# Kernel tuning notes

Measured on AMD Instinct MI355X. Metric: run time of the kernel, lower is better.

Reference implementation:

```python
import jax, jax.numpy as jnp
import numpy as np

K, D, Q, N = 32, 256, 16, 4096
LOG2PI = float(np.log(2.0 * np.pi))


def setup_inputs() -> dict:
    key = jax.random.key(0)
    k1, k2, k3, k4 = jax.random.split(key, 4)
    X = jax.random.normal(k1, (N, D), dtype=jnp.float32)
    log_pi = jnp.full((K,), -np.log(K), dtype=jnp.float32)  # uniform mixture weights
    mu = 0.1 * jax.random.normal(k2, (K, D), dtype=jnp.float32)
    Lambda = 0.1 * jax.random.normal(k3, (K, D, Q), dtype=jnp.float32)
    log_psi = np.float32(np.log(0.01)) + 0.1 * jax.random.normal(k4, (K, D), dtype=jnp.float32)
    return {"X": X, "log_pi": log_pi, "mu": mu, "Lambda": Lambda, "log_psi": log_psi}


def reference(X, log_pi, mu, Lambda, log_psi):
    """MFA e_step: per-component Gaussian log-prob with C_k = L_k L_k^T + diag(psi_k) + jitter.
    Returns (log_resp_norm [N,K], log_likelihood [N]) — same math as the torch loop, batched over K."""
    d = X.shape[1]
    psi = jnp.exp(log_psi) + 1e-6                       # [K,D]
    C = jnp.einsum('kdq,keq->kde', Lambda, Lambda)       # [K,D,D] low-rank part
    C = C + jnp.eye(d, dtype=X.dtype) * (psi + 1e-5)[:, None, :]  # add diag(psi) + 1e-5 jitter
    chol = jnp.linalg.cholesky(C)                        # [K,D,D]
    diff = X[None, :, :] - mu[:, None, :]                # [K,N,D]
    # solve chol @ y = diff^T  (batched lower-triangular solve)
    y = jax.scipy.linalg.solve_triangular(chol, diff.transpose(0, 2, 1), lower=True)  # [K,D,N]
    maha = jnp.sum(y * y, axis=1)                        # [K,N]
    logdet = 2.0 * jnp.sum(jnp.log(jnp.diagonal(chol, axis1=1, axis2=2)), axis=1)  # [K]
    log_prob = -0.5 * (maha + d * LOG2PI + logdet[:, None])  # [K,N]
    log_resps = log_prob.T + log_pi[None, :]             # [N,K]
    log_likelihood = jax.scipy.special.logsumexp(log_resps, axis=1)  # [N]
    log_resp_norm = log_resps - log_likelihood[:, None]
    return log_resp_norm, log_likelihood
```

## Files before the change

### kernel.cpp

```cpp
#include <hip/hip_runtime.h>
#include <math.h>

#define KC 32
#define DD 256
#define QQ 16
#define NPTS 4096
#define NROW 8
#define LOG2PI_F 1.8378770664093453f

typedef unsigned short ushort_t;

#define OFF_U    0
#define OFF_LOGC 512
#define OFF_HB   544

__device__ __forceinline__ ushort_t f2bf(float f) {
    union { float f; unsigned int u; } c; c.f = f;
    unsigned int u = c.u;
    return (ushort_t)((u + 0x7FFFu + ((u >> 16) & 1u)) >> 16);
}
__device__ __forceinline__ float bf2f(ushort_t h) {
    union { unsigned int u; float f; } c; c.u = ((unsigned int)h) << 16;
    return c.f;
}

using short8 = __attribute__((ext_vector_type(8))) short;
using f32x4  = __attribute__((ext_vector_type(4))) float;

#define PSTR 260
__global__ __launch_bounds__(256) void precompute_kernel(
    const float* __restrict__ log_pi, const float* __restrict__ mu,
    const float* __restrict__ Lambda, const float* __restrict__ log_psi,
    float* __restrict__ ws)
{
    __shared__ __align__(16) float sLamT[QQ * PSTR];
    __shared__ __align__(16) float sLhatT[QQ * PSTR];
    __shared__ __align__(16) float sMu[DD];
    __shared__ float sM[QQ * 17];
    __shared__ float sL[QQ * 17];
    __shared__ float sY[QQ * 17];
    __shared__ float sCol[QQ];
    __shared__ float sPart[8];
    __shared__ float sScal[2];

    const int k = blockIdx.x;
    const int tid = threadIdx.x;
    const int lane = tid & 63;
    const int wave = tid >> 6;
    ushort_t* hb = (ushort_t*)(ws + OFF_HB);
    const int d = tid;

    float Psi  = expf(log_psi[k * DD + d]) + 1.1e-5f;
    float vinv = 1.0f / Psi;
    float mud  = mu[k * DD + d];
    float wv   = vinv * mud;
    hb[(512 + k) * DD + d] = f2bf(vinv);
    hb[(544 + k) * DD + d] = f2bf(wv);
    sMu[d] = mud;
    float logPsi = logf(Psi);
    float ckp = wv * mud;

    float lam[QQ];
    const float4* lrow = reinterpret_cast<const float4*>(Lambda + (size_t)(k * DD + d) * QQ);
#pragma unroll
    for (int i = 0; i < 4; ++i) {
        float4 t = lrow[i];
        lam[4 * i + 0] = t.x; lam[4 * i + 1] = t.y;
        lam[4 * i + 2] = t.z; lam[4 * i + 3] = t.w;
    }
#pragma unroll
    for (int q = 0; q < QQ; ++q) {
        float lh = lam[q] * vinv;
        sLamT[q * PSTR + d]  = lam[q];
        sLhatT[q * PSTR + d] = lh;
        hb[(k * QQ + q) * DD + d] = f2bf(lh);
    }

    float r0 = logPsi, r1 = ckp;
#pragma unroll
    for (int off = 32; off >= 1; off >>= 1) {
        r0 += __shfl_down(r0, off);
        r1 += __shfl_down(r1, off);
    }
    if ((tid & 63) == 0) { sPart[wave] = r0; sPart[4 + wave] = r1; }
    __syncthreads();
    if (tid == 0) {
        sScal[0] = sPart[0] + sPart[1] + sPart[2] + sPart[3];
        sScal[1] = sPart[4] + sPart[5] + sPart[6] + sPart[7];
    }

    {
        int q = tid >> 4, r = tid & 15;
        const float4* aq = reinterpret_cast<const float4*>(sLhatT + q * PSTR);
        const float4* br = reinterpret_cast<const float4*>(sLamT + r * PSTR);
        float acc = 0.f;
#pragma unroll
        for (int i = 0; i < DD / 4; ++i) {
            float4 a = aq[i], b = br[i];
            acc += a.x * b.x + a.y * b.y + a.z * b.z + a.w * b.w;
        }
        sM[q * 17 + r] = acc + ((q == r) ? 1.0f : 0.0f);
    }
    __syncthreads();
    if (tid < QQ) {
        const float4* aq = reinterpret_cast<const float4*>(sLhatT + tid * PSTR);
        const float4* bm = reinterpret_cast<const float4*>(sMu);
        float acc = 0.f;
#pragma unroll
        for (int i = 0; i < DD / 4; ++i) {
            float4 a = aq[i], b = bm[i];
            acc += a.x * b.x + a.y * b.y + a.z * b.z + a.w * b.w;
        }
        ws[OFF_U + k * QQ + tid] = acc;
    }

    if (wave == 0 && lane < QQ) {
        const int r = lane;
        float m[QQ], l[QQ];
#pragma unroll
        for (int c = 0; c < QQ; ++c) m[c] = sM[r * 17 + c];
#pragma unroll
        for (int j = 0; j < QQ; ++j) {
            float djj = __shfl(m[j], j);
            float rinv = 1.0f / sqrtf(djj);
            l[j] = m[j] * rinv;
            sCol[r] = l[j];
#pragma unroll
            for (int c = 0; c < QQ; ++c)
                if (c > j) m[c] -= l[j] * sCol[c];
        }
#pragma unroll
        for (int j = 0; j < QQ; ++j) sL[r * 17 + j] = l[j];
        float dl = logf(l[r]);
        dl += __shfl_xor(dl, 1); dl += __shfl_xor(dl, 2);
        dl += __shfl_xor(dl, 4); dl += __shfl_xor(dl, 8);
        if (r == 0) sPart[1] = dl;
    }
    __syncthreads();

    if (wave == 0 && lane < QQ) {
        const int c = lane;
        float y[QQ];
#pragma unroll
        for (int j = 0; j < QQ; ++j) {
            float acc = (j == c) ? 1.0f : 0.0f;
#pragma unroll
            for (int i = 0; i < QQ; ++i)
                if (i < j) acc -= sL[j * 17 + i] * y[i];
            y[j] = acc / sL[j * 17 + j];
        }
#pragma unroll
        for (int j = 0; j < QQ; ++j) sY[j * 17 + c] = y[j];
    }
    __syncthreads();

    {
        int q = tid >> 4, r = tid & 15;
        float acc = 0.f;
#pragma unroll
        for (int j = 0; j < QQ; ++j) acc += sY[j * 17 + q] * sY[j * 17 + r];
        hb[(576 + k) * DD + tid] = f2bf(acc);
    }
    if (tid == 0) {
        float logdet = sScal[0] + 2.0f * sPart[1];
        ws[OFF_LOGC + k] = log_pi[k] - 0.5f * ((float)DD * LOG2PI_F + logdet)
                         - 0.5f * sScal[1];
    }
}

#define SXH 264
#define TSTR 520
#define QSTR 68
#define SRS 36

__global__ __launch_bounds__(512, 2) void main_kernel(
    const float* __restrict__ X, const float* __restrict__ ws,
    float* __restrict__ out)
{
    const int tid  = threadIdx.x;
    const int lane = tid & 63;
    const int wave = tid >> 6;
    const int n0   = blockIdx.x * NROW;
    const ushort_t* hB = (const ushort_t*)(ws + OFF_HB);

    __shared__ __align__(16) ushort_t xh[16 * SXH];
    __shared__ __align__(16) ushort_t sT[NROW * TSTR];
    __shared__ __align__(16) float    sQS[NROW * QSTR];
    __shared__ float sU[512];
    __shared__ float sLogc[KC];
    __shared__ float sR[NROW * SRS];
    __shared__ float sLse[NROW];

    {
        const float4* gx = reinterpret_cast<const float4*>(X + (size_t)n0 * DD);
        int row = tid >> 6, d4 = tid & 63;
        float4 v = gx[tid];
        *reinterpret_cast<ushort4*>(&xh[row * SXH + d4 * 4]) =
            make_ushort4(f2bf(v.x), f2bf(v.y), f2bf(v.z), f2bf(v.w));
        int zr = 8 + (tid >> 6), zc = (tid & 63) * 4;
        *reinterpret_cast<ushort4*>(&xh[zr * SXH + zc]) = make_ushort4(0, 0, 0, 0);
        sU[tid] = ws[OFF_U + tid];
        if (tid < KC) sLogc[tid] = ws[OFF_LOGC + tid];
    }
    __syncthreads();

    {
        const int arow = lane & 15;
        const int quad = lane >> 4;
        short8 a[8];
        const ushort_t* ab = xh + arow * SXH + quad * 8;
#pragma unroll
        for (int ks = 0; ks < 8; ++ks) a[ks] = *reinterpret_cast<const short8*>(ab + ks * 32);

#pragma unroll
        for (int i = 0; i < 4; ++i) {
            const int tile = wave * 4 + i;
            const ushort_t* gB = hB + (size_t)(tile * 16 + arow) * DD + quad * 8;
            f32x4 acc = (f32x4){0.f, 0.f, 0.f, 0.f};
#pragma unroll
            for (int ks = 0; ks < 8; ++ks)
                acc = __builtin_amdgcn_mfma_f32_16x16x32_bf16(
                    a[ks], *reinterpret_cast<const short8*>(gB + ks * 32), acc, 0, 0, 0);
            float uu = sU[tile * 16 + arow];
#pragma unroll
            for (int r = 0; r < 4; ++r) {
                int rr = quad * 4 + r;
                if (rr < NROW) sT[rr * TSTR + tile * 16 + arow] = f2bf(acc[r] - uu);
            }
        }
        if (wave < 4) {
            short8 aa[8];
            if (wave < 2) {
#pragma unroll
                for (int ks = 0; ks < 8; ++ks) {
                    short8 sq;
#pragma unroll
                    for (int e = 0; e < 8; ++e) {
                        float xf = bf2f((ushort_t)a[ks][e]);
                        sq[e] = (short)f2bf(xf * xf);
                    }
                    aa[ks] = sq;
                }
            } else {
#pragma unroll
                for (int ks = 0; ks < 8; ++ks) aa[ks] = a[ks];
            }
            const ushort_t* gB = hB + (size_t)(512 + wave * 16 + arow) * DD + quad * 8;
            f32x4 acc = (f32x4){0.f, 0.f, 0.f, 0.f};
#pragma unroll
            for (int ks = 0; ks < 8; ++ks)
                acc = __builtin_amdgcn_mfma_f32_16x16x32_bf16(
                    aa[ks], *reinterpret_cast<const short8*>(gB + ks * 32), acc, 0, 0, 0);
            const int col = (wave & 1) * 16 + arow + ((wave >> 1) & 1) * 32;
#pragma unroll
            for (int r = 0; r < 4; ++r) {
                int rr = quad * 4 + r;
                if (rr < NROW) sQS[rr * QSTR + col] = acc[r];
            }
        }
    }
    __syncthreads();

    {
        const int half = tid & 1;
        const int row  = (tid >> 1) & 7;
        const int c    = (tid >> 4) & 31;
        float t[16];
        {
            const ushort_t* tp = sT + row * TSTR + c * 16;
            short8 t0 = *reinterpret_cast<const short8*>(tp);
            short8 t1 = *reinterpret_cast<const short8*>(tp + 8);
#pragma unroll
            for (int e = 0; e < 8; ++e) {
                t[e]     = bf2f((ushort_t)t0[e]);
                t[8 + e] = bf2f((ushort_t)t1[e]);
            }
        }
        const ushort_t* mp = hB + (size_t)(576 + c) * DD + half * 128;
        float corr = 0.f;
#pragma unroll
        for (int q = 0; q < 8; ++q) {
            short8 m0 = *reinterpret_cast<const short8*>(mp + q * 16);
            short8 m1 = *reinterpret_cast<const short8*>(mp + q * 16 + 8);
            float inner = 0.f;
#pragma unroll
            for (int e = 0; e < 8; ++e)
                inner += bf2f((ushort_t)m0[e]) * t[e] + bf2f((ushort_t)m1[e]) * t[8 + e];
            corr += t[half * 8 + q] * inner;
        }
        corr += __shfl_xor(corr, 1);
        if (half == 0) {
            float qx = sQS[row * QSTR + c];
            float sx = sQS[row * QSTR + 32 + c];
            sR[row * SRS + c] = sLogc[c] - 0.5f * (qx - 2.0f * sx - corr);
        }
    }
    __syncthreads();

    if (tid < NROW) {
        float m = -INFINITY;
#pragma unroll
        for (int c = 0; c < KC; ++c) m = fmaxf(m, sR[tid * SRS + c]);
        float sum = 0.f;
#pragma unroll
        for (int c = 0; c < KC; ++c) sum += expf(sR[tid * SRS + c] - m);
        float lse = m + logf(sum);
        sLse[tid] = lse;
        out[(size_t)NPTS * KC + n0 + tid] = lse;
    }
    __syncthreads();
    if (tid < NROW * 8) {
        int r = tid >> 3, i = tid & 7;
        float lse = sLse[r];
        float4 v = *reinterpret_cast<const float4*>(sR + r * SRS + i * 4);
        float4 o = make_float4(v.x - lse, v.y - lse, v.z - lse, v.w - lse);
        *reinterpret_cast<float4*>(out + (size_t)(n0 + r) * KC + i * 4) = o;
    }
}

extern "C" void kernel_launch(void* const* d_in, const int* in_sizes, int n_in,
                              void* d_out, int out_size, void* d_ws, size_t ws_size,
                              hipStream_t stream)
{
    (void)in_sizes; (void)n_in; (void)out_size; (void)ws_size;
    const float* X       = (const float*)d_in[0];
    const float* log_pi  = (const float*)d_in[1];
    const float* mu      = (const float*)d_in[2];
    const float* Lambda  = (const float*)d_in[3];
    const float* log_psi = (const float*)d_in[4];
    float* out = (float*)d_out;
    float* ws  = (float*)d_ws;

    precompute_kernel<<<dim3(KC), dim3(256), 0, stream>>>(log_pi, mu, Lambda, log_psi, ws);
    main_kernel<<<dim3(NPTS / NROW), dim3(512), 0, stream>>>(X, ws, out);
}
```

Measured before the change: 94.97 us.

## Process 16 points per block and use MFMA for precompute Gram products

The main kernel now handles 16 rows per block instead of 8, so the 16-row MFMA tiles are fully used rather than half padded with zeros, and the grid is halved. The correction stage loops over two components per thread to cover the doubled work. The precompute kernel stores Lambda, Lambda/psi and mu as bf16 in shared memory and computes the 16x16 Gram matrix and the u vector with MFMA instead of scalar fp32 dot products. This adds bf16 rounding to the precompute and halves the number of blocks, which lowers occupancy and parallelism.

```diff
diff --git a/kernel.cpp b/kernel.cpp
--- a/kernel.cpp
+++ b/kernel.cpp
@@ -5,7 +5,7 @@
 #define DD 256
 #define QQ 16
 #define NPTS 4096
-#define NROW 8
+#define NROW 16
 #define LOG2PI_F 1.8378770664093453f
 
 typedef unsigned short ushort_t;
@@ -27,15 +27,15 @@
 using short8 = __attribute__((ext_vector_type(8))) short;
 using f32x4  = __attribute__((ext_vector_type(4))) float;
 
-#define PSTR 260
+#define HSTR 264
 __global__ __launch_bounds__(256) void precompute_kernel(
     const float* __restrict__ log_pi, const float* __restrict__ mu,
     const float* __restrict__ Lambda, const float* __restrict__ log_psi,
     float* __restrict__ ws)
 {
-    __shared__ __align__(16) float sLamT[QQ * PSTR];
-    __shared__ __align__(16) float sLhatT[QQ * PSTR];
-    __shared__ __align__(16) float sMu[DD];
+    __shared__ __align__(16) ushort_t lamH[QQ * HSTR];
+    __shared__ __align__(16) ushort_t lhatH[QQ * HSTR];
+    __shared__ __align__(16) ushort_t smuH[QQ * HSTR];
     __shared__ float sM[QQ * 17];
     __shared__ float sL[QQ * 17];
     __shared__ float sY[QQ * 17];
@@ -56,24 +56,38 @@
     float wv   = vinv * mud;
     hb[(512 + k) * DD + d] = f2bf(vinv);
     hb[(544 + k) * DD + d] = f2bf(wv);
-    sMu[d] = mud;
+    smuH[d] = f2bf(mud);
     float logPsi = logf(Psi);
     float ckp = wv * mud;
 
-    float lam[QQ];
-    const float4* lrow = reinterpret_cast<const float4*>(Lambda + (size_t)(k * DD + d) * QQ);
+    {
+        const float4* lrow = reinterpret_cast<const float4*>(Lambda + (size_t)(k * DD + d) * QQ);
+#pragma unroll
+        for (int i = 0; i < 4; ++i) {
+            float4 t = lrow[i];
+            float l0 = t.x, l1 = t.y, l2 = t.z, l3 = t.w;
+            int q = 4 * i;
+            lamH[(q + 0) * HSTR + d] = f2bf(l0);
+            lamH[(q + 1) * HSTR + d] = f2bf(l1);
+            lamH[(q + 2) * HSTR + d] = f2bf(l2);
+            lamH[(q + 3) * HSTR + d] = f2bf(l3);
+            ushort_t h0 = f2bf(l0 * vinv), h1 = f2bf(l1 * vinv);
+            ushort_t h2 = f2bf(l2 * vinv), h3 = f2bf(l3 * vinv);
+            lhatH[(q + 0) * HSTR + d] = h0;
+            lhatH[(q + 1) * HSTR + d] = h1;
+            lhatH[(q + 2) * HSTR + d] = h2;
+            lhatH[(q + 3) * HSTR + d] = h3;
+            hb[(k * QQ + q + 0) * DD + d] = h0;
+            hb[(k * QQ + q + 1) * DD + d] = h1;
+            hb[(k * QQ + q + 2) * DD + d] = h2;
+            hb[(k * QQ + q + 3) * DD + d] = h3;
+        }
+    }
 #pragma unroll
     for (int i = 0; i < 4; ++i) {
-        float4 t = lrow[i];
-        lam[4 * i + 0] = t.x; lam[4 * i + 1] = t.y;
-        lam[4 * i + 2] = t.z; lam[4 * i + 3] = t.w;
-    }
-#pragma unroll
-    for (int q = 0; q < QQ; ++q) {
-        float lh = lam[q] * vinv;
-        sLamT[q * PSTR + d]  = lam[q];
-        sLhatT[q * PSTR + d] = lh;
-        hb[(k * QQ + q) * DD + d] = f2bf(lh);
+        int idx = tid + i * 256;
+        if (idx < 990)
+            *reinterpret_cast<ushort4*>(smuH + HSTR + idx * 4) = make_ushort4(0, 0, 0, 0);
     }
 
     float r0 = logPsi, r1 = ckp;
@@ -89,30 +103,34 @@
         sScal[1] = sPart[4] + sPart[5] + sPart[6] + sPart[7];
     }
 
-    {
-        int q = tid >> 4, r = tid & 15;
-        const float4* aq = reinterpret_cast<const float4*>(sLhatT + q * PSTR);
-        const float4* br = reinterpret_cast<const float4*>(sLamT + r * PSTR);
-        float acc = 0.f;
-#pragma unroll
-        for (int i = 0; i < DD / 4; ++i) {
-            float4 a = aq[i], b = br[i];
-            acc += a.x * b.x + a.y * b.y + a.z * b.z + a.w * b.w;
-        }
-        sM[q * 17 + r] = acc + ((q == r) ? 1.0f : 0.0f);
-    }
-    __syncthreads();
-    if (tid < QQ) {
-        const float4* aq = reinterpret_cast<const float4*>(sLhatT + tid * PSTR);
-        const float4* bm = reinterpret_cast<const float4*>(sMu);
-        float acc = 0.f;
-#pragma unroll
-        for (int i = 0; i < DD / 4; ++i) {
-            float4 a = aq[i], b = bm[i];
-            acc += a.x * b.x + a.y * b.y + a.z * b.z + a.w * b.w;
-        }
-        ws[OFF_U + k * QQ + tid] = acc;
-    }
+    if (wave == 0) {
+        const int arow = lane & 15;
+        const int quad = lane >> 4;
+        const ushort_t* pa = lhatH + arow * HSTR + quad * 8;
+        const ushort_t* pl = lamH  + arow * HSTR + quad * 8;
+        const ushort_t* pm = smuH  + arow * HSTR + quad * 8;
+        f32x4 accM = (f32x4){0.f, 0.f, 0.f, 0.f};
+        f32x4 accU = (f32x4){0.f, 0.f, 0.f, 0.f};
+#pragma unroll
+        for (int ks = 0; ks < 8; ++ks) {
+            short8 a = *reinterpret_cast<const short8*>(pa + ks * 32);
+            accM = __builtin_amdgcn_mfma_f32_16x16x32_bf16(
+                a, *reinterpret_cast<const short8*>(pl + ks * 32), accM, 0, 0, 0);
+            accU = __builtin_amdgcn_mfma_f32_16x16x32_bf16(
+                a, *reinterpret_cast<const short8*>(pm + ks * 32), accU, 0, 0, 0);
+        }
+#pragma unroll
+        for (int reg = 0; reg < 4; ++reg) {
+            int q = quad * 4 + reg;
+            sM[q * 17 + arow] = accM[reg] + ((q == arow) ? 1.0f : 0.0f);
+        }
+        if (arow == 0) {
+#pragma unroll
+            for (int reg = 0; reg < 4; ++reg)
+                ws[OFF_U + k * QQ + quad * 4 + reg] = accU[reg];
+        }
+    }
+    __syncthreads();
 
     if (wave == 0 && lane < QQ) {
         const int r = lane;
@@ -183,7 +201,7 @@
     const int n0   = blockIdx.x * NROW;
     const ushort_t* hB = (const ushort_t*)(ws + OFF_HB);
 
-    __shared__ __align__(16) ushort_t xh[16 * SXH];
+    __shared__ __align__(16) ushort_t xh[NROW * SXH];
     __shared__ __align__(16) ushort_t sT[NROW * TSTR];
     __shared__ __align__(16) float    sQS[NROW * QSTR];
     __shared__ float sU[512];
@@ -193,12 +211,14 @@
 
     {
         const float4* gx = reinterpret_cast<const float4*>(X + (size_t)n0 * DD);
-        int row = tid >> 6, d4 = tid & 63;
-        float4 v = gx[tid];
-        *reinterpret_cast<ushort4*>(&xh[row * SXH + d4 * 4]) =
-            make_ushort4(f2bf(v.x), f2bf(v.y), f2bf(v.z), f2bf(v.w));
-        int zr = 8 + (tid >> 6), zc = (tid & 63) * 4;
-        *reinterpret_cast<ushort4*>(&xh[zr * SXH + zc]) = make_ushort4(0, 0, 0, 0);
+#pragma unroll
+        for (int i = 0; i < 2; ++i) {
+            int f = tid + i * 512;
+            int row = f >> 6, d4 = f & 63;
+            float4 v = gx[f];
+            *reinterpret_cast<ushort4*>(&xh[row * SXH + d4 * 4]) =
+                make_ushort4(f2bf(v.x), f2bf(v.y), f2bf(v.z), f2bf(v.w));
+        }
         sU[tid] = ws[OFF_U + tid];
         if (tid < KC) sLogc[tid] = ws[OFF_LOGC + tid];
     }
@@ -223,10 +243,8 @@
                     a[ks], *reinterpret_cast<const short8*>(gB + ks * 32), acc, 0, 0, 0);
             float uu = sU[tile * 16 + arow];
 #pragma unroll
-            for (int r = 0; r < 4; ++r) {
-                int rr = quad * 4 + r;
-                if (rr < NROW) sT[rr * TSTR + tile * 16 + arow] = f2bf(acc[r] - uu);
-            }
+            for (int r = 0; r < 4; ++r)
+                sT[(quad * 4 + r) * TSTR + tile * 16 + arow] = f2bf(acc[r] - uu);
         }
         if (wave < 4) {
             short8 aa[8];
@@ -253,46 +271,48 @@
                     aa[ks], *reinterpret_cast<const short8*>(gB + ks * 32), acc, 0, 0, 0);
             const int col = (wave & 1) * 16 + arow + ((wave >> 1) & 1) * 32;
 #pragma unroll
-            for (int r = 0; r < 4; ++r) {
-                int rr = quad * 4 + r;
-                if (rr < NROW) sQS[rr * QSTR + col] = acc[r];
+            for (int r = 0; r < 4; ++r)
+                sQS[(quad * 4 + r) * QSTR + col] = acc[r];
+        }
+    }
+    __syncthreads();
+
+    {
+        const int half = tid & 1;
+        const int row  = (tid >> 1) & 15;
+        const int c0   = tid >> 5;
+#pragma unroll
+        for (int ci = 0; ci < 2; ++ci) {
+            const int c = c0 + ci * 16;
+            float t[16];
+            {
+                const ushort_t* tp = sT + row * TSTR + c * 16;
+                short8 t0 = *reinterpret_cast<const short8*>(tp);
+                short8 t1 = *reinterpret_cast<const short8*>(tp + 8);
+#pragma unroll
+                for (int e = 0; e < 8; ++e) {
+                    t[e]     = bf2f((ushort_t)t0[e]);
+                    t[8 + e] = bf2f((ushort_t)t1[e]);
+                }
             }
-        }
-    }
-    __syncthreads();
-
-    {
-        const int half = tid & 1;
-        const int row  = (tid >> 1) & 7;
-        const int c    = (tid >> 4) & 31;
-        float t[16];
-        {
-            const ushort_t* tp = sT + row * TSTR + c * 16;
-            short8 t0 = *reinterpret_cast<const short8*>(tp);
-            short8 t1 = *reinterpret_cast<const short8*>(tp + 8);
-#pragma unroll
-            for (int e = 0; e < 8; ++e) {
-                t[e]     = bf2f((ushort_t)t0[e]);
-                t[8 + e] = bf2f((ushort_t)t1[e]);
+            const ushort_t* mp = hB + (size_t)(576 + c) * DD + half * 128;
+            float corr = 0.f;
+#pragma unroll
+            for (int q = 0; q < 8; ++q) {
+                short8 m0 = *reinterpret_cast<const short8*>(mp + q * 16);
+                short8 m1 = *reinterpret_cast<const short8*>(mp + q * 16 + 8);
+                float inner = 0.f;
+#pragma unroll
+                for (int e = 0; e < 8; ++e)
+                    inner += bf2f((ushort_t)m0[e]) * t[e] + bf2f((ushort_t)m1[e]) * t[8 + e];
+                corr += t[half * 8 + q] * inner;
             }
-        }
-        const ushort_t* mp = hB + (size_t)(576 + c) * DD + half * 128;
-        float corr = 0.f;
-#pragma unroll
-        for (int q = 0; q < 8; ++q) {
-            short8 m0 = *reinterpret_cast<const short8*>(mp + q * 16);
-            short8 m1 = *reinterpret_cast<const short8*>(mp + q * 16 + 8);
-            float inner = 0.f;
-#pragma unroll
-            for (int e = 0; e < 8; ++e)
-                inner += bf2f((ushort_t)m0[e]) * t[e] + bf2f((ushort_t)m1[e]) * t[8 + e];
-            corr += t[half * 8 + q] * inner;
-        }
-        corr += __shfl_xor(corr, 1);
-        if (half == 0) {
-            float qx = sQS[row * QSTR + c];
-            float sx = sQS[row * QSTR + 32 + c];
-            sR[row * SRS + c] = sLogc[c] - 0.5f * (qx - 2.0f * sx - corr);
+            corr += __shfl_xor(corr, 1);
+            if (half == 0) {
+                float qx = sQS[row * QSTR + c];
+                float sx = sQS[row * QSTR + 32 + c];
+                sR[row * SRS + c] = sLogc[c] - 0.5f * (qx - 2.0f * sx - corr);
+            }
         }
     }
     __syncthreads();
```

After: 84.90 us. 10.6% less time.
